# Optimization experiments

Hardware: AMD Instinct MI355X
Metric: run time of the kernel (lower is better)

The kernel has to match this reference:

```python
import jax, jax.numpy as jnp
import numpy as np

LN_EPS = 1e-5


def layer_norm(x, g, b):
    m = jnp.mean(x, axis=-1, keepdims=True)
    v = jnp.mean(jnp.square(x - m), axis=-1, keepdims=True)
    return (x - m) * jax.lax.rsqrt(v + LN_EPS) * g + b


def sym_norm(A):
    # D^{-1/2} (A + I) D^{-1/2}
    N = A.shape[0]
    Ah = A + jnp.eye(N, dtype=A.dtype)
    d = jnp.sum(Ah, axis=-1)
    dinv = jax.lax.rsqrt(jnp.maximum(d, 1e-12))
    return Ah * dinv[:, None] * dinv[None, :]


def gru_layer(xs, Wih, Whh, bih, bhh):
    # xs: (BN, T, Din) -> ys: (BN, T, H). PyTorch GRU cell math.
    BN, T, _ = xs.shape
    H = Whh.shape[1]
    x_proj = xs @ Wih.T + bih  # (BN, T, 3H), precompute input projections

    def step(h, xp):
        hp = h @ Whh.T + bhh
        xr, xz, xn = jnp.split(xp, 3, axis=-1)
        hr, hz, hn = jnp.split(hp, 3, axis=-1)
        r = jax.nn.sigmoid(xr + hr)
        z = jax.nn.sigmoid(xz + hz)
        n = jnp.tanh(xn + r * hn)
        h_new = (1.0 - z) * n + z * h
        return h_new, h_new

    h0 = jnp.zeros((BN, H), xs.dtype)
    _, ys = jax.lax.scan(step, h0, jnp.swapaxes(x_proj, 0, 1))
    return jnp.swapaxes(ys, 0, 1)


def amscf_forward(x, A, FSP, DSP,
                  E1, E2, fus_W, fus_b, fus_v, beta1, beta2,
                  gcn_W1, gcn_b1, ln1_g, ln1_b, gcn_W2, gcn_b2, ln2_g, ln2_b,
                  gru_Wih0, gru_Whh0, gru_bih0, gru_bhh0,
                  gru_Wih1, gru_Whh1, gru_bih1, gru_bhh1,
                  att_w, fc1_W, fc1_b, fc2_W, fc2_b):
    B, T, N, _ = x.shape
    Hor = fc2_W.shape[0]

    # ImprovedAdjacency: blend A with adaptive node-embedding adjacency
    Aadp = jax.nn.softmax(jax.nn.relu(E1 @ E2.T), axis=-1)
    IA = 0.5 * A + 0.5 * Aadp

    # fuse_with_A with learned gates
    w1 = jax.nn.sigmoid(beta1)
    w2 = jax.nn.sigmoid(beta2)
    C1 = w1 * A + (1.0 - w1) * FSP
    C2 = w2 * A + (1.0 - w2) * DSP

    # TransposeAttentionFusion: graph-level attention over the 3 candidate graphs
    Gs = jnp.stack([IA, C1, C2], axis=0)  # (3, N, N)
    sc = jnp.mean(jnp.tanh(Gs @ fus_W.T + fus_b) @ fus_v, axis=-1)  # (3,)
    alpha = jax.nn.softmax(sc)
    MG = jnp.einsum('k,knm->nm', alpha, Gs)

    S_hat = sym_norm(MG)  # (N, N)

    # TwoLayerGCN over all (B, T) at once: act(LN(S X W1)) -> LN(S h W2)
    xf = x.reshape(B * T, N, 1)
    h = jnp.einsum('mn,bnc->bmc', S_hat, xf) @ gcn_W1 + gcn_b1
    h = jax.nn.relu(layer_norm(h, ln1_g, ln1_b))
    g = jnp.einsum('mn,bnc->bmc', S_hat, h) @ gcn_W2 + gcn_b2
    g = layer_norm(g, ln2_g, ln2_b)  # (B*T, N, C)

    C = g.shape[-1]
    # Faithful to original: raw view of (B, T, N, C) into (B*N, T, C)
    H_seq = g.reshape(B, T, N, C).reshape(B * N, T, C)

    out = gru_layer(H_seq, gru_Wih0, gru_Whh0, gru_bih0, gru_bhh0)
    out = gru_layer(out, gru_Wih1, gru_Whh1, gru_bih1, gru_bhh1)  # (BN, T, Hg)

    # SoftAttentionPooling over time
    score = out @ att_w  # (BN, T)
    att = jax.nn.softmax(score, axis=1)
    ctx = jnp.einsum('bt,bth->bh', att, out)

    hfc = jax.nn.gelu(ctx @ fc1_W.T + fc1_b)
    dlt = hfc @ fc2_W.T + fc2_b  # (BN, Hor); dropout is identity at eval
    return jnp.transpose(dlt.reshape(B, N, Hor), (0, 2, 1))  # (B, Hor, N)


def setup_inputs() -> dict:
    B, T, N, Hor = 32, 12, 1000, 12
    Cin, Ch, Cout, Hg, Da, De = 1, 96, 96, 192, 32, 10
    key = jax.random.key(0)
    ks = jax.random.split(key, 32)
    f32 = jnp.float32

    def nrm(k, shape, scale):
        return jax.random.normal(k, shape, dtype=f32) * scale

    inp = {
        'x': jax.random.normal(ks[0], (B, T, N, Cin), dtype=f32),
        'A': jax.random.uniform(ks[1], (N, N), dtype=f32),
        'FSP': jax.random.uniform(ks[2], (N, N), dtype=f32),
        'DSP': jax.random.uniform(ks[3], (N, N), dtype=f32),
        'E1': nrm(ks[4], (N, De), 0.1),
        'E2': nrm(ks[5], (N, De), 0.1),
        'fus_W': nrm(ks[6], (Da, N), 1.0 / np.sqrt(N)),
        'fus_b': jnp.zeros((Da,), f32),
        'fus_v': nrm(ks[7], (Da,), 1.0 / np.sqrt(Da)),
        'beta1': jnp.float32(0.5),
        'beta2': jnp.float32(0.5),
        'gcn_W1': nrm(ks[8], (Cin, Ch), 1.0 / np.sqrt(Cin)),
        'gcn_b1': jnp.zeros((Ch,), f32),
        'ln1_g': jnp.ones((Ch,), f32),
        'ln1_b': jnp.zeros((Ch,), f32),
        'gcn_W2': nrm(ks[9], (Ch, Cout), 1.0 / np.sqrt(Ch)),
        'gcn_b2': jnp.zeros((Cout,), f32),
        'ln2_g': jnp.ones((Cout,), f32),
        'ln2_b': jnp.zeros((Cout,), f32),
        'gru_Wih0': nrm(ks[10], (3 * Hg, Cout), 1.0 / np.sqrt(Hg)),
        'gru_Whh0': nrm(ks[11], (3 * Hg, Hg), 1.0 / np.sqrt(Hg)),
        'gru_bih0': jnp.zeros((3 * Hg,), f32),
        'gru_bhh0': jnp.zeros((3 * Hg,), f32),
        'gru_Wih1': nrm(ks[12], (3 * Hg, Hg), 1.0 / np.sqrt(Hg)),
        'gru_Whh1': nrm(ks[13], (3 * Hg, Hg), 1.0 / np.sqrt(Hg)),
        'gru_bih1': jnp.zeros((3 * Hg,), f32),
        'gru_bhh1': jnp.zeros((3 * Hg,), f32),
        'att_w': nrm(ks[14], (Hg,), 1.0 / np.sqrt(Hg)),
        'fc1_W': nrm(ks[15], (Hg, Hg), 1.0 / np.sqrt(Hg)),
        'fc1_b': jnp.zeros((Hg,), f32),
        'fc2_W': nrm(ks[16], (Hor, Hg), 1.0 / np.sqrt(Hg)),
        'fc2_b': jnp.zeros((Hor,), f32),
    }
    return inp


def reference(x, A, FSP, DSP, E1, E2, fus_W, fus_b, fus_v, beta1, beta2,
              gcn_W1, gcn_b1, ln1_g, ln1_b, gcn_W2, gcn_b2, ln2_g, ln2_b,
              gru_Wih0, gru_Whh0, gru_bih0, gru_bhh0,
              gru_Wih1, gru_Whh1, gru_bih1, gru_bhh1,
              att_w, fc1_W, fc1_b, fc2_W, fc2_b):
    return amscf_forward(x, A, FSP, DSP, E1, E2, fus_W, fus_b, fus_v, beta1, beta2,
                         gcn_W1, gcn_b1, ln1_g, ln1_b, gcn_W2, gcn_b2, ln2_g, ln2_b,
                         gru_Wih0, gru_Whh0, gru_bih0, gru_bhh0,
                         gru_Wih1, gru_Whh1, gru_bih1, gru_bhh1,
                         att_w, fc1_W, fc1_b, fc2_W, fc2_b)
```

## Files before the change

### kernel.cpp

```cpp
#include <hip/hip_runtime.h>

typedef unsigned short u16;
typedef unsigned int u32;
typedef __attribute__((ext_vector_type(8))) short short8;
typedef __attribute__((ext_vector_type(4))) float float4v;

#define DEV static __device__ __forceinline__

DEV float bf2f(u16 u) { u32 x = ((u32)u) << 16; float f; __builtin_memcpy(&f, &x, 4); return f; }
DEV u16 f2bf(float f) {
  u32 u; __builtin_memcpy(&u, &f, 4);
  u = (u + 0x7fffu + ((u >> 16) & 1u)) >> 16;
  return (u16)u;
}
DEV float sigm(float x) { return 1.f / (1.f + __expf(-x)); }

DEV void gl16(const u16* g, u16* l) {
  __builtin_amdgcn_global_load_lds(
      (const __attribute__((address_space(1))) void*)g,
      (__attribute__((address_space(3))) void*)l, 16, 0, 0);
}

template <int OMODE>
__launch_bounds__(256)
__global__ void gemm_nt(const u16* __restrict__ A, int lda,
                        const u16* __restrict__ B, int ldb,
                        void* __restrict__ Cp, int ldc,
                        int M, int N, int K,
                        const float* __restrict__ bias)
{
  constexpr int PK = 40;
  __shared__ u16 As[128 * PK];
  __shared__ u16 Bs[64 * PK];

  const int tid  = threadIdx.x;
  const int m0   = blockIdx.y * 128;
  const int n0   = blockIdx.x * 64;
  const int wid  = tid >> 6;
  const int lane = tid & 63;
  const int l15  = lane & 15;
  const int quad = lane >> 4;
  const int wm   = (wid >> 1) * 64;
  const int wn   = (wid & 1) * 32;

  float4v acc[4][2];
  const float4v fz = {0.f, 0.f, 0.f, 0.f};
#pragma unroll
  for (int i = 0; i < 4; i++)
#pragma unroll
    for (int j = 0; j < 2; j++) acc[i][j] = fz;

  const int arow = tid >> 2;
  const int akc  = tid & 3;

  const int kt_count = (K + 31) / 32;
  for (int kt = 0; kt < kt_count; ++kt) {
    const int k0 = kt * 32 + akc * 8;
    const bool kok = (k0 < K);
    uint4 av0 = make_uint4(0, 0, 0, 0), av1 = av0, bv = av0;
    int ra = m0 + arow;
    if (kok && ra < M)        av0 = *(const uint4*)(A + (size_t)ra * lda + k0);
    if (kok && ra + 64 < M)   av1 = *(const uint4*)(A + (size_t)(ra + 64) * lda + k0);
    int rb = n0 + arow;
    if (kok && rb < N)        bv  = *(const uint4*)(B + (size_t)rb * ldb + k0);

    __syncthreads();
    *(uint4*)&As[arow * PK + akc * 8]        = av0;
    *(uint4*)&As[(arow + 64) * PK + akc * 8] = av1;
    *(uint4*)&Bs[arow * PK + akc * 8]        = bv;
    __syncthreads();

    short8 af[4], bfr[2];
#pragma unroll
    for (int i = 0; i < 4; i++)
      af[i] = *(const short8*)&As[(wm + i * 16 + l15) * PK + quad * 8];
#pragma unroll
    for (int j = 0; j < 2; j++)
      bfr[j] = *(const short8*)&Bs[(wn + j * 16 + l15) * PK + quad * 8];
#pragma unroll
    for (int i = 0; i < 4; i++)
#pragma unroll
      for (int j = 0; j < 2; j++)
        acc[i][j] = __builtin_amdgcn_mfma_f32_16x16x32_bf16(af[i], bfr[j], acc[i][j], 0, 0, 0);
  }

#pragma unroll
  for (int i = 0; i < 4; i++)
#pragma unroll
    for (int j = 0; j < 2; j++)
#pragma unroll
      for (int e = 0; e < 4; e++) {
        int r = m0 + wm + i * 16 + quad * 4 + e;
        int c = n0 + wn + j * 16 + l15;
        if (r < M && c < N) {
          float v = acc[i][j][e];
          if (OMODE == 0) ((float*)Cp)[(size_t)r * ldc + c] = v;
          else {
            float a = v + bias[c];
            float t = tanhf(0.7978845608028654f * (a + 0.044715f * a * a * a));
            ((float*)Cp)[(size_t)r * ldc + c] = 0.5f * a * (1.f + t);
          }
        }
      }
}

__launch_bounds__(256)
__global__ void k_bigemm(const u16* __restrict__ A,
                         const u16* __restrict__ B,
                         const float* __restrict__ b2, const float* __restrict__ g2,
                         const float* __restrict__ be2,
                         u16* __restrict__ Gg)
{
  __shared__ u16 As[128 * 32];
  __shared__ u16 Bs[96 * 32];
  __shared__ float stats[2][2][128];

  const int tid  = threadIdx.x;
  const int bid  = blockIdx.x;
  const int xcd  = bid & 7;
  const int jj   = bid >> 3;
  const int m0   = (jj & 7) * 128;
  const int rt   = xcd + 8 * (jj >> 3);

  const int wid  = tid >> 6;
  const int lane = tid & 63;
  const int l15  = lane & 15;
  const int quad = lane >> 4;
  const int wm   = (wid >> 1) * 64;
  const int wn   = (wid & 1) * 48;
  const int wni  = wid & 1;

  const int srow = lane >> 2;
  const int skc  = ((lane & 3) ^ ((lane >> 3) & 3)) * 8;

  const u16* agp0 = A + (size_t)(m0 + wid * 16 + srow) * 1024 + skc;
  const u16* agp1 = agp0 + (size_t)64 * 1024;
  const u16* bgp0 = B + (size_t)(rt * 96 + wid * 16 + srow) * 1024 + skc;
  const u16* bgp1 = bgp0 + (size_t)64 * 1024;
  u16* asl0 = &As[(wid * 16) * 32];
  u16* asl1 = &As[(64 + wid * 16) * 32];
  u16* bsl0 = &Bs[(wid * 16) * 32];
  u16* bsl1 = &Bs[(64 + wid * 16) * 32];

  float4v acc[4][3];
  const float4v fz = {0.f, 0.f, 0.f, 0.f};
#pragma unroll
  for (int i = 0; i < 4; i++)
#pragma unroll
    for (int j = 0; j < 3; j++) acc[i][j] = fz;

  const int swa = (quad ^ ((l15 >> 1) & 3)) * 8;

  for (int kt = 0; kt < 32; ++kt) {
    const int ko = kt * 32;
    gl16(agp0 + ko, asl0);
    gl16(agp1 + ko, asl1);
    gl16(bgp0 + ko, bsl0);
    if (wid < 2) gl16(bgp1 + ko, bsl1);
    __syncthreads();
    short8 af[4], bf[3];
#pragma unroll
    for (int i = 0; i < 4; i++)
      af[i] = *(const short8*)&As[(wm + i * 16 + l15) * 32 + swa];
#pragma unroll
    for (int j = 0; j < 3; j++)
      bf[j] = *(const short8*)&Bs[(wn + j * 16 + l15) * 32 + swa];
#pragma unroll
    for (int i = 0; i < 4; i++)
#pragma unroll
      for (int j = 0; j < 3; j++)
        acc[i][j] = __builtin_amdgcn_mfma_f32_16x16x32_bf16(af[i], bf[j], acc[i][j], 0, 0, 0);
    __syncthreads();
  }

  float b2v[3], g2v[3], bev[3];
#pragma unroll
  for (int j = 0; j < 3; j++) {
    int c = wn + j * 16 + l15;
    b2v[j] = b2[c]; g2v[j] = g2[c]; bev[j] = be2[c];
  }
#pragma unroll
  for (int i = 0; i < 4; i++)
#pragma unroll
    for (int e = 0; e < 4; e++) {
      float s = 0.f, ss = 0.f;
#pragma unroll
      for (int j = 0; j < 3; j++) {
        float v = acc[i][j][e] + b2v[j];
        acc[i][j][e] = v;
        s += v; ss += v * v;
      }
      s += __shfl_xor(s, 1); ss += __shfl_xor(ss, 1);
      s += __shfl_xor(s, 2); ss += __shfl_xor(ss, 2);
      s += __shfl_xor(s, 4); ss += __shfl_xor(ss, 4);
      s += __shfl_xor(s, 8); ss += __shfl_xor(ss, 8);
      if (l15 == 0) {
        int rl = wm + i * 16 + quad * 4 + e;
        stats[wni][0][rl] = s;
        stats[wni][1][rl] = ss;
      }
    }
  __syncthreads();
#pragma unroll
  for (int i = 0; i < 4; i++)
#pragma unroll
    for (int e = 0; e < 4; e++) {
      int rl = wm + i * 16 + quad * 4 + e;
      int m = m0 + rl;
      if (m < 1000) {
        float ts  = stats[0][0][rl] + stats[1][0][rl];
        float tss = stats[0][1][rl] + stats[1][1][rl];
        float mean = ts * (1.f / 96.f);
        float var  = tss * (1.f / 96.f) - mean * mean;
        float isd  = rsqrtf(var + 1e-5f);
#pragma unroll
        for (int j = 0; j < 3; j++) {
          int c = wn + j * 16 + l15;
          Gg[(size_t)rt * 96000 + (size_t)m * 96 + c] =
              f2bf((acc[i][j][e] - mean) * isd * g2v[j] + bev[j]);
        }
      }
    }
}

template <int KX, bool POOL>
__launch_bounds__(256)
__global__ void k_gru(const u16* __restrict__ Xin, int ldx,
                      const u16* __restrict__ Win,
                      const u16* __restrict__ Hin,
                      const u16* __restrict__ Whh,
                      const float* __restrict__ bih, const float* __restrict__ bhh,
                      u16* __restrict__ Hout,
                      const float* __restrict__ att_w,
                      float* __restrict__ score_acc,
                      float* __restrict__ score_zero,
                      const u16* __restrict__ Hpool,
                      const float* __restrict__ score_rd,
                      const float* __restrict__ Mrd, const float* __restrict__ Lrd,
                      float* __restrict__ Mwr, float* __restrict__ Lwr,
                      float* __restrict__ Nvp,
                      int t0, int pm)
{
  __shared__ u16 As[128 * 64];
  __shared__ u16 Bs[96 * 64];
  const int tid  = threadIdx.x;
  const int m0   = blockIdx.y * 128;
  const int c0   = blockIdx.x * 32;
  const int wid  = tid >> 6;
  const int lane = tid & 63;
  const int l15  = lane & 15;
  const int quad = lane >> 4;
  const int wm   = wid * 32;

  if (!POOL && pm) {
#pragma unroll
    for (int k = 0; k < 16; k++) {
      int idx = k * 256 + tid;
      int ql = idx >> 5, cl = idx & 31;
      int q = m0 + ql, c = c0 + cl;
      size_t nidx = (size_t)q * 192 + c;
      float s = score_rd[q];
      float hnew = bf2f(Hpool[nidx]);
      float so, wnf, prev;
      if (pm == 1) { so = 0.f; wnf = 1.f; prev = 0.f; }
      else {
        float Mo = Mrd[q];
        float Mn = fmaxf(Mo, s);
        so = __expf(Mo - Mn); wnf = __expf(s - Mn);
        prev = Nvp[nidx];
      }
      Nvp[nidx] = prev * so + wnf * hnew;
    }
    if (blockIdx.x == 0 && tid < 128) {
      int q = m0 + tid;
      float s = score_rd[q];
      if (pm == 1) { Mwr[q] = s; Lwr[q] = 1.f; }
      else {
        float Mo = Mrd[q], Mn = fmaxf(Mo, s);
        Mwr[q] = Mn;
        Lwr[q] = Lrd[q] * __expf(Mo - Mn) + __expf(s - Mn);
      }
    }
  }
  if (POOL && blockIdx.x == 0 && tid < 128) score_zero[m0 + tid] = 0.f;

  const int srow8 = lane >> 3;
  const int sw8   = ((lane & 7) ^ srow8) * 8;
  const int srow4 = lane >> 2;
  const int sw4   = ((lane & 3) ^ ((lane >> 3) & 3)) * 8;

  float4v aR[2][2], aZ[2][2], aXN[2][2], aHN[2][2];
  const float4v fz = {0.f, 0.f, 0.f, 0.f};
#pragma unroll
  for (int i = 0; i < 2; i++)
#pragma unroll
    for (int j = 0; j < 2; j++) { aR[i][j] = fz; aZ[i][j] = fz; aXN[i][j] = fz; aHN[i][j] = fz; }

  if (KX == 96) {
    const u16* ax0 = Xin + (size_t)(m0 + wid * 16 + srow4) * ldx + sw4;
    const u16* ax1 = Xin + (size_t)(m0 + 64 + wid * 16 + srow4) * ldx + sw4;
    const int b0 = wid * 16 + srow4;
    const u16* bx0 = Win + (size_t)((b0 >> 5) * 192 + c0 + (b0 & 31)) * 96 + sw4;
    const int b1 = 64 + wid * 16 + srow4;
    const u16* bx1 = Win + (size_t)(384 + c0 + (b1 & 31)) * 96 + sw4;
    u16* asl0 = &As[(wid * 16) * 32];
    u16* asl1 = &As[(64 + wid * 16) * 32];
    u16* bsl0 = &Bs[(wid * 16) * 32];
    u16* bsl1 = &Bs[(64 + wid * 16) * 32];
    const int swa = (quad ^ ((l15 >> 1) & 3)) * 8;
#pragma unroll
    for (int kt = 0; kt < 3; ++kt) {
      const int ko = kt * 32;
      gl16(ax0 + ko, asl0); gl16(ax1 + ko, asl1);
      gl16(bx0 + ko, bsl0);
      if (wid < 2) gl16(bx1 + ko, bsl1);
      __syncthreads();
      short8 af[2], bR[2], bZ[2], bN[2];
#pragma unroll
      for (int i = 0; i < 2; i++)
        af[i] = *(const short8*)&As[(wm + i * 16 + l15) * 32 + swa];
#pragma unroll
      for (int j = 0; j < 2; j++) {
        bR[j] = *(const short8*)&Bs[(j * 16 + l15) * 32 + swa];
        bZ[j] = *(const short8*)&Bs[(32 + j * 16 + l15) * 32 + swa];
        bN[j] = *(const short8*)&Bs[(64 + j * 16 + l15) * 32 + swa];
      }
#pragma unroll
      for (int i = 0; i < 2; i++)
#pragma unroll
        for (int j = 0; j < 2; j++) {
          aR[i][j]  = __builtin_amdgcn_mfma_f32_16x16x32_bf16(af[i], bR[j], aR[i][j], 0, 0, 0);
          aZ[i][j]  = __builtin_amdgcn_mfma_f32_16x16x32_bf16(af[i], bZ[j], aZ[i][j], 0, 0, 0);
          aXN[i][j] = __builtin_amdgcn_mfma_f32_16x16x32_bf16(af[i], bN[j], aXN[i][j], 0, 0, 0);
        }
      __syncthreads();
    }
  } else {
    const u16* abase = Xin + (size_t)(m0 + wid * 8 + srow8) * 192 + sw8;
    const u16* bbase = Win + (size_t)(c0 + wid * 8 + srow8) * 192 + sw8;
#pragma unroll
    for (int kt = 0; kt < 3; ++kt) {
      const int ko = kt * 64;
#pragma unroll
      for (int c = 0; c < 4; c++)
        gl16(abase + (size_t)c * 32 * 192 + ko, &As[(c * 32 + wid * 8) * 64]);
#pragma unroll
      for (int c = 0; c < 3; c++)
        gl16(bbase + (size_t)c * 192 * 192 + ko, &Bs[(c * 32 + wid * 8) * 64]);
      __syncthreads();
#pragma unroll
      for (int k32 = 0; k32 < 2; k32++) {
        const int swr = ((quad + 4 * k32) ^ (l15 & 7)) * 8;
        short8 af[2], bR[2], bZ[2], bN[2];
#pragma unroll
        for (int i = 0; i < 2; i++)
          af[i] = *(const short8*)&As[(wm + i * 16 + l15) * 64 + swr];
#pragma unroll
        for (int j = 0; j < 2; j++) {
          bR[j] = *(const short8*)&Bs[(j * 16 + l15) * 64 + swr];
          bZ[j] = *(const short8*)&Bs[(32 + j * 16 + l15) * 64 + swr];
          bN[j] = *(const short8*)&Bs[(64 + j * 16 + l15) * 64 + swr];
        }
#pragma unroll
        for (int i = 0; i < 2; i++)
#pragma unroll
          for (int j = 0; j < 2; j++) {
            aR[i][j]  = __builtin_amdgcn_mfma_f32_16x16x32_bf16(af[i], bR[j], aR[i][j], 0, 0, 0);
            aZ[i][j]  = __builtin_amdgcn_mfma_f32_16x16x32_bf16(af[i], bZ[j], aZ[i][j], 0, 0, 0);
            aXN[i][j] = __builtin_amdgcn_mfma_f32_16x16x32_bf16(af[i], bN[j], aXN[i][j], 0, 0, 0);
          }
      }
      __syncthreads();
    }
  }
  if (!t0) {
    const u16* abase = Hin + (size_t)(m0 + wid * 8 + srow8) * 192 + sw8;
    const u16* bbase = Whh + (size_t)(c0 + wid * 8 + srow8) * 192 + sw8;
#pragma unroll
    for (int kt = 0; kt < 3; ++kt) {
      const int ko = kt * 64;
#pragma unroll
      for (int c = 0; c < 4; c++)
        gl16(abase + (size_t)c * 32 * 192 + ko, &As[(c * 32 + wid * 8) * 64]);
#pragma unroll
      for (int c = 0; c < 3; c++)
        gl16(bbase + (size_t)c * 192 * 192 + ko, &Bs[(c * 32 + wid * 8) * 64]);
      __syncthreads();
#pragma unroll
      for (int k32 = 0; k32 < 2; k32++) {
        const int swr = ((quad + 4 * k32) ^ (l15 & 7)) * 8;
        short8 af[2], bR[2], bZ[2], bN[2];
#pragma unroll
        for (int i = 0; i < 2; i++)
          af[i] = *(const short8*)&As[(wm + i * 16 + l15) * 64 + swr];
#pragma unroll
        for (int j = 0; j < 2; j++) {
          bR[j] = *(const short8*)&Bs[(j * 16 + l15) * 64 + swr];
          bZ[j] = *(const short8*)&Bs[(32 + j * 16 + l15) * 64 + swr];
          bN[j] = *(const short8*)&Bs[(64 + j * 16 + l15) * 64 + swr];
        }
#pragma unroll
        for (int i = 0; i < 2; i++)
#pragma unroll
          for (int j = 0; j < 2; j++) {
            aR[i][j]  = __builtin_amdgcn_mfma_f32_16x16x32_bf16(af[i], bR[j], aR[i][j], 0, 0, 0);
            aZ[i][j]  = __builtin_amdgcn_mfma_f32_16x16x32_bf16(af[i], bZ[j], aZ[i][j], 0, 0, 0);
            aHN[i][j] = __builtin_amdgcn_mfma_f32_16x16x32_bf16(af[i], bN[j], aHN[i][j], 0, 0, 0);
          }
      }
      __syncthreads();
    }
  }

  float ps[2][4];
  if (POOL) {
#pragma unroll
    for (int i = 0; i < 2; i++)
#pragma unroll
      for (int e = 0; e < 4; e++) ps[i][e] = 0.f;
  }
#pragma unroll
  for (int j = 0; j < 2; ++j) {
    const int c = c0 + j * 16 + l15;
    const float brz = bih[c] + bhh[c];
    const float bzz = bih[192 + c] + bhh[192 + c];
    const float bxn = bih[384 + c];
    const float bhn = bhh[384 + c];
    const float aw  = POOL ? att_w[c] : 0.f;
#pragma unroll
    for (int i = 0; i < 2; ++i)
#pragma unroll
      for (int e = 0; e < 4; ++e) {
        const int row = m0 + wm + i * 16 + quad * 4 + e;
        float rg  = sigm(aR[i][j][e] + brz);
        float zg  = sigm(aZ[i][j][e] + bzz);
        float hnv = bhn + (t0 ? 0.f : aHN[i][j][e]);
        float ng  = tanhf(aXN[i][j][e] + bxn + rg * hnv);
        float hold = t0 ? 0.f : bf2f(Hin[(size_t)row * 192 + c]);
        float hnew = (1.f - zg) * ng + zg * hold;
        Hout[(size_t)row * 192 + c] = f2bf(hnew);
        if (POOL) ps[i][e] += hnew * aw;
      }
  }
  if (POOL) {
#pragma unroll
    for (int i = 0; i < 2; ++i)
#pragma unroll
      for (int e = 0; e < 4; ++e) {
        float v = ps[i][e];
        v += __shfl_xor(v, 1); v += __shfl_xor(v, 2);
        v += __shfl_xor(v, 4); v += __shfl_xor(v, 8);
        if (l15 == 0) atomicAdd(&score_acc[m0 + wm + i * 16 + quad * 4 + e], v);
      }
  }
}

__launch_bounds__(256)
__global__ void k_pool(const u16* __restrict__ H, const float* __restrict__ score_rd,
                       const float* __restrict__ Mrd, const float* __restrict__ Lrd,
                       float* __restrict__ Lwr, float* __restrict__ Nv)
{
  const int base = blockIdx.x * 1536;
  const int tid  = threadIdx.x;
#pragma unroll
  for (int k = 0; k < 6; k++) {
    const int idx = base + tid + k * 256;
    const int q = idx / 192;
    const float s = score_rd[q];
    const float Mo = Mrd[q];
    const float Mn = fmaxf(Mo, s);
    const float so = __expf(Mo - Mn);
    const float wn = __expf(s - Mn);
    Nv[idx] = Nv[idx] * so + wn * bf2f(H[idx]);
  }
  if (tid < 8) {
    const int q = blockIdx.x * 8 + tid;
    const float s = score_rd[q];
    const float Mo = Mrd[q];
    const float Mn = fmaxf(Mo, s);
    Lwr[q] = Lrd[q] * __expf(Mo - Mn) + __expf(s - Mn);
  }
}

__launch_bounds__(256)
__global__ void k_h2gemm(const float* __restrict__ yt, const float4* __restrict__ cwpk,
                         const u16* __restrict__ W2s, const float* __restrict__ consts,
                         u16* __restrict__ h2t)
{
  constexpr int PK = 40;
  __shared__ u16 As[128 * PK];
  __shared__ u16 Bs[96 * PK];
  __shared__ u16 Ts[96 * 136];

  const int tid  = threadIdx.x;
  const int m0   = blockIdx.x * 128;
  const int wid  = tid >> 6;
  const int lane = tid & 63;
  const int l15  = lane & 15;
  const int quad = lane >> 4;
  const int wm   = (wid >> 1) * 64;
  const int wn   = (wid & 1) * 48;

  const float P = consts[0], Q = consts[1], VW = consts[2], CWB = consts[3], VB = consts[4];

  const int arow = tid >> 2;
  const int akc  = tid & 3;

  float yv[2], mu[2], iv[2];
#pragma unroll
  for (int rr = 0; rr < 2; rr++) {
    int i = m0 + arow + rr * 64;
    int r = i / 1000, n = i - r * 1000;
    float y = yt[n * 384 + r];
    yv[rr] = y;
    mu[rr] = y * P + Q;
    iv[rr] = rsqrtf(y * y * VW + 2.f * y * CWB + VB + 1e-5f);
  }

  float4v acc[4][3];
  const float4v fz = {0.f, 0.f, 0.f, 0.f};
#pragma unroll
  for (int i = 0; i < 4; i++)
#pragma unroll
    for (int j = 0; j < 3; j++) acc[i][j] = fz;

  uint4 asave[2][3];
  const bool has2 = (arow < 32);

  for (int kt = 0; kt < 6; ++kt) {
    const int k0 = kt * 32 + akc * 8;
    uint4 av[2];
    if (kt < 3) {
#pragma unroll
      for (int rr = 0; rr < 2; rr++) {
        u16 hb[8];
#pragma unroll
        for (int e = 0; e < 8; e++) {
          float4 cw = cwpk[k0 + e];
          float t = yv[rr] * cw.x + cw.y - mu[rr];
          float h = fmaxf(t * iv[rr] * cw.z + cw.w, 0.f);
          hb[e] = f2bf(h);
        }
        __builtin_memcpy(&av[rr], hb, 16);
        asave[rr][kt] = av[rr];
      }
    } else {
      av[0] = asave[0][kt - 3];
      av[1] = asave[1][kt - 3];
    }
    uint4 bv0 = *(const uint4*)(W2s + (size_t)arow * 192 + k0);
    uint4 bv1 = make_uint4(0, 0, 0, 0);
    if (has2) bv1 = *(const uint4*)(W2s + (size_t)(arow + 64) * 192 + k0);

    __syncthreads();
    *(uint4*)&As[arow * PK + akc * 8]        = av[0];
    *(uint4*)&As[(arow + 64) * PK + akc * 8] = av[1];
    *(uint4*)&Bs[arow * PK + akc * 8]        = bv0;
    if (has2) *(uint4*)&Bs[(arow + 64) * PK + akc * 8] = bv1;
    __syncthreads();

    short8 af[4], bfr[3];
#pragma unroll
    for (int i = 0; i < 4; i++)
      af[i] = *(const short8*)&As[(wm + i * 16 + l15) * PK + quad * 8];
#pragma unroll
    for (int j = 0; j < 3; j++)
      bfr[j] = *(const short8*)&Bs[(wn + j * 16 + l15) * PK + quad * 8];
#pragma unroll
    for (int i = 0; i < 4; i++)
#pragma unroll
      for (int j = 0; j < 3; j++)
        acc[i][j] = __builtin_amdgcn_mfma_f32_16x16x32_bf16(af[i], bfr[j], acc[i][j], 0, 0, 0);
  }

#pragma unroll
  for (int i = 0; i < 4; i++)
#pragma unroll
    for (int j = 0; j < 3; j++)
#pragma unroll
      for (int e = 0; e < 4; e++) {
        int rowl = wm + i * 16 + quad * 4 + e;
        int c2   = wn + j * 16 + l15;
        Ts[c2 * 136 + rowl] = f2bf(acc[i][j][e]);
      }
  __syncthreads();
#pragma unroll
  for (int u = tid; u < 1536; u += 256) {
    int c2 = u >> 4, ch = u & 15;
    int iidx0 = m0 + ch * 8;
    int r = iidx0 / 1000, n0 = iidx0 - r * 1000;
    *(uint4*)(h2t + (size_t)(r * 96 + c2) * 1024 + n0) = *(const uint4*)&Ts[c2 * 136 + ch * 8];
  }
}

__launch_bounds__(256)
__global__ void k_prep(const float* x, const float* fus_W,
                       const float* Wih0, const float* Whh0,
                       const float* Wih1, const float* Whh1,
                       const float* gcn_W1, const float* gcn_b1,
                       const float* gcn_W2, const float* ln1g, const float* ln1b,
                       u16* xbf, u16* fusWbf, u16* Wih0b, u16* Whh0b, u16* Wih1b, u16* Whh1b,
                       u16* W2s, float4* cwpk, float* consts)
{
  long o = (long)blockIdx.x * 256 + threadIdx.x;
  if (o < 384000) xbf[o] = f2bf(x[o]);
  else if ((o -= 384000) < 32000) fusWbf[o] = f2bf(fus_W[o]);
  else if ((o -= 32000) < 55296)  Wih0b[o] = f2bf(Wih0[o]);
  else if ((o -= 55296) < 110592) Whh0b[o] = f2bf(Whh0[o]);
  else if ((o -= 110592) < 110592) Wih1b[o] = f2bf(Wih1[o]);
  else if ((o -= 110592) < 110592) Whh1b[o] = f2bf(Whh1[o]);
  else if ((o -= 110592) < 9216) {
    int c2 = (int)o / 96, c = (int)o - c2 * 96;
    float wv = gcn_W2[c * 96 + c2];
    u16 hi = f2bf(wv);
    u16 lo = f2bf(wv - bf2f(hi));
    W2s[c2 * 192 + c] = hi;
    W2s[c2 * 192 + 96 + c] = lo;
  }
  else if ((o -= 9216) < 96) {
    int c = (int)o;
    float4 cw;
    cw.x = gcn_W1[c]; cw.y = gcn_b1[c]; cw.z = ln1g[c]; cw.w = ln1b[c];
    cwpk[c] = cw;
  }
  if (blockIdx.x == 0 && threadIdx.x == 0) {
    float sw = 0, sb = 0, sww = 0, swb = 0, sbb = 0;
    for (int c = 0; c < 96; c++) {
      float wv = gcn_W1[c], b = gcn_b1[c];
      sw += wv; sb += b; sww += wv * wv; swb += wv * b; sbb += b * b;
    }
    float P = sw / 96.f, Q = sb / 96.f;
    consts[0] = P; consts[1] = Q;
    consts[2] = sww / 96.f - P * P;
    consts[3] = swb / 96.f - P * Q;
    consts[4] = sbb / 96.f - Q * Q;
  }
}

__launch_bounds__(256)
__global__ void k_zero(u16* __restrict__ h2t, float* __restrict__ score0,
                       float* __restrict__ score1)
{
  int idx = blockIdx.x * 256 + threadIdx.x;
  if (idx < 110592) {
    int row = idx / 3, p = idx - row * 3;
    *(uint4*)(h2t + (size_t)row * 1024 + 1000 + p * 8) = make_uint4(0, 0, 0, 0);
  } else if ((idx -= 110592) < 32000) {
    score0[idx] = 0.f;
  } else if ((idx -= 32000) < 32000) {
    score1[idx] = 0.f;
  }
}

__launch_bounds__(256)
__global__ void k_w1split(const float* __restrict__ fc1W, u16* __restrict__ w1s)
{
  int idx = blockIdx.x * 256 + threadIdx.x;
  if (idx >= 192 * 192) return;
  int n = idx / 192, k = idx - n * 192;
  float w = fc1W[idx];
  u16 hi = f2bf(w);
  u16 lo = f2bf(w - bf2f(hi));
  w1s[(size_t)n * 576 + k]       = hi;
  w1s[(size_t)n * 576 + 192 + k] = lo;
  w1s[(size_t)n * 576 + 384 + k] = hi;
}

__launch_bounds__(256)
__global__ void k_adjrow(const float* __restrict__ A, const float* __restrict__ FSP,
                         const float* __restrict__ DSP, const float* __restrict__ E1,
                         const float* __restrict__ E2,
                         const float* beta1, const float* beta2,
                         u16* __restrict__ G, float* __restrict__ rowsums)
{
  __shared__ float z[1000];
  __shared__ float red[256];
  const int n = blockIdx.x, tid = threadIdx.x;

  float e1r[10];
#pragma unroll
  for (int d = 0; d < 10; d++) e1r[d] = E1[n * 10 + d];

  float lmax = -1e30f;
  for (int m = tid; m < 1000; m += 256) {
    float s = 0;
#pragma unroll
    for (int d = 0; d < 10; d++) s += e1r[d] * E2[m * 10 + d];
    s = fmaxf(s, 0.f);
    z[m] = s;
    lmax = fmaxf(lmax, s);
  }
  red[tid] = lmax; __syncthreads();
  for (int st = 128; st > 0; st >>= 1) { if (tid < st) red[tid] = fmaxf(red[tid], red[tid + st]); __syncthreads(); }
  const float mx = red[0]; __syncthreads();

  float lsum = 0;
  for (int m = tid; m < 1000; m += 256) { float e = __expf(z[m] - mx); z[m] = e; lsum += e; }
  red[tid] = lsum; __syncthreads();
  for (int st = 128; st > 0; st >>= 1) { if (tid < st) red[tid] += red[tid + st]; __syncthreads(); }
  const float inv = 1.f / red[0]; __syncthreads();

  const float w1 = sigm(beta1[0]);
  const float w2 = sigm(beta2[0]);
  float s0 = 0, s1 = 0, s2 = 0;
  for (int m = tid; m < 1000; m += 256) {
    float aadp = z[m] * inv;
    float a = A[n * 1000 + m], f = FSP[n * 1000 + m], dd = DSP[n * 1000 + m];
    float g0 = 0.5f * a + 0.5f * aadp;
    float g1 = w1 * a + (1.f - w1) * f;
    float g2 = w2 * a + (1.f - w2) * dd;
    G[0 * 1000000 + n * 1000 + m] = f2bf(g0);
    G[1 * 1000000 + n * 1000 + m] = f2bf(g1);
    G[2 * 1000000 + n * 1000 + m] = f2bf(g2);
    s0 += g0; s1 += g1; s2 += g2;
  }
  red[tid] = s0; __syncthreads();
  for (int st = 128; st > 0; st >>= 1) { if (tid < st) red[tid] += red[tid + st]; __syncthreads(); }
  if (tid == 0) rowsums[n] = red[0];
  __syncthreads();
  red[tid] = s1; __syncthreads();
  for (int st = 128; st > 0; st >>= 1) { if (tid < st) red[tid] += red[tid + st]; __syncthreads(); }
  if (tid == 0) rowsums[1000 + n] = red[0];
  __syncthreads();
  red[tid] = s2; __syncthreads();
  for (int st = 128; st > 0; st >>= 1) { if (tid < st) red[tid] += red[tid + st]; __syncthreads(); }
  if (tid == 0) rowsums[2000 + n] = red[0];
}

__launch_bounds__(256)
__global__ void k_sc(const float* __restrict__ P, const float* fus_b, const float* fus_v, float* sc)
{
  __shared__ float red[256];
  const int k = blockIdx.x, tid = threadIdx.x;
  float local = 0;
  for (int n = tid; n < 1000; n += 256) {
    const float* p = P + (size_t)(k * 1000 + n) * 32;
    float s = 0;
#pragma unroll
    for (int a = 0; a < 32; a++) s += tanhf(p[a] + fus_b[a]) * fus_v[a];
    local += s;
  }
  red[tid] = local; __syncthreads();
  for (int st = 128; st > 0; st >>= 1) { if (tid < st) red[tid] += red[tid + st]; __syncthreads(); }
  if (tid == 0) sc[k] = red[0] * (1.f / 1000.f);
}

__launch_bounds__(256)
__global__ void k_alpha(const float* sc, const float* rowsums, float* alpha_out, float* dinv)
{
  __shared__ float al[3];
  const int tid = threadIdx.x;
  if (tid == 0) {
    float m = fmaxf(sc[0], fmaxf(sc[1], sc[2]));
    float e0 = __expf(sc[0] - m), e1 = __expf(sc[1] - m), e2 = __expf(sc[2] - m);
    float inv = 1.f / (e0 + e1 + e2);
    al[0] = e0 * inv; al[1] = e1 * inv; al[2] = e2 * inv;
    alpha_out[0] = al[0]; alpha_out[1] = al[1]; alpha_out[2] = al[2];
  }
  __syncthreads();
  const float a0 = al[0], a1 = al[1], a2 = al[2];
  for (int n = tid; n < 1000; n += 256) {
    float d = a0 * rowsums[n] + a1 * rowsums[1000 + n] + a2 * rowsums[2000 + n] + 1.0f;
    dinv[n] = rsqrtf(fmaxf(d, 1e-12f));
  }
}

__launch_bounds__(256)
__global__ void k_shat(const u16* __restrict__ G, const float* alpha, const float* dinv,
                       u16* __restrict__ S)
{
  int idx = blockIdx.x * 256 + threadIdx.x;
  if (idx >= 1024000) return;
  int i = idx >> 10, j = idx & 1023;
  u16 val = 0;
  if (j < 1000) {
    const float a0 = alpha[0], a1 = alpha[1], a2 = alpha[2];
    int g = i * 1000 + j;
    float mg = a0 * bf2f(G[g]) + a1 * bf2f(G[1000000 + g]) + a2 * bf2f(G[2000000 + g]);
    if (i == j) mg += 1.0f;
    val = f2bf(mg * dinv[i] * dinv[j]);
  }
  S[(size_t)i * 1024 + j] = val;
}

__launch_bounds__(256)
__global__ void k_ctxsplit(const float* __restrict__ Nv, const float* __restrict__ Lbuf,
                           u16* __restrict__ ctxs)
{
  const int i = blockIdx.x * 256 + threadIdx.x;
  if (i >= 32000 * 192) return;
  const int q = i / 192, c = i - q * 192;
  float v = Nv[i] / Lbuf[q];
  u16 hi = f2bf(v);
  u16 lo = f2bf(v - bf2f(hi));
  u16* row = ctxs + (size_t)q * 576;
  row[c] = hi; row[192 + c] = hi; row[384 + c] = lo;
}

__launch_bounds__(192)
__global__ void k_fc2(const float* __restrict__ hfc, const float* __restrict__ fc2W,
                      const float* __restrict__ fc2b, float* __restrict__ out)
{
  __shared__ float w2S[12][193];
  __shared__ float hS[16][193];
  const int tid = threadIdx.x;
  const int q0 = blockIdx.x * 16;
  for (int idx = tid; idx < 12 * 192; idx += 192) {
    int o = idx / 192, k = idx - o * 192;
    w2S[o][k] = fc2W[idx];
  }
  for (int idx = tid; idx < 16 * 192; idx += 192) {
    int qq = idx / 192, k = idx - qq * 192;
    hS[qq][k] = hfc[(size_t)(q0 + qq) * 192 + k];
  }
  __syncthreads();
  const int qq = tid / 12, o = tid - qq * 12;
  float acc = fc2b[o];
#pragma unroll 8
  for (int k = 0; k < 192; k++) acc += hS[qq][k] * w2S[o][k];
  const int q = q0 + qq;
  const int b = q / 1000, node = q - b * 1000;
  out[(size_t)b * 12000 + o * 1000 + node] = acc;
}

extern "C" void kernel_launch(void* const* d_in, const int* in_sizes, int n_in,
                              void* d_out, int out_size, void* d_ws, size_t ws_size,
                              hipStream_t stream)
{
  const float* x     = (const float*)d_in[0];
  const float* A     = (const float*)d_in[1];
  const float* FSP   = (const float*)d_in[2];
  const float* DSP   = (const float*)d_in[3];
  const float* E1    = (const float*)d_in[4];
  const float* E2    = (const float*)d_in[5];
  const float* fus_W = (const float*)d_in[6];
  const float* fus_b = (const float*)d_in[7];
  const float* fus_v = (const float*)d_in[8];
  const float* beta1 = (const float*)d_in[9];
  const float* beta2 = (const float*)d_in[10];
  const float* gcn_W1= (const float*)d_in[11];
  const float* gcn_b1= (const float*)d_in[12];
  const float* ln1g  = (const float*)d_in[13];
  const float* ln1b  = (const float*)d_in[14];
  const float* gcn_W2= (const float*)d_in[15];
  const float* gcn_b2= (const float*)d_in[16];
  const float* ln2g  = (const float*)d_in[17];
  const float* ln2b  = (const float*)d_in[18];
  const float* Wih0  = (const float*)d_in[19];
  const float* Whh0  = (const float*)d_in[20];
  const float* bih0  = (const float*)d_in[21];
  const float* bhh0  = (const float*)d_in[22];
  const float* Wih1  = (const float*)d_in[23];
  const float* Whh1  = (const float*)d_in[24];
  const float* bih1  = (const float*)d_in[25];
  const float* bhh1  = (const float*)d_in[26];
  const float* att_w = (const float*)d_in[27];
  const float* fc1W  = (const float*)d_in[28];
  const float* fc1b  = (const float*)d_in[29];
  const float* fc2W  = (const float*)d_in[30];
  const float* fc2b  = (const float*)d_in[31];
  float* out = (float*)d_out;

  char* w = (char*)d_ws;
  auto alloc = [&](size_t bytes) -> char* {
    char* p = w;
    w += (bytes + 255) & ~(size_t)255;
    return p;
  };

  float* consts  = (float*)alloc(8 * 4);
  float* scp     = (float*)alloc(3 * 4);
  float* alphap  = (float*)alloc(3 * 4);
  float* rowsums = (float*)alloc(3000 * 4);
  float* dinvp   = (float*)alloc(1000 * 4);
  u16*   Gbuf    = (u16*)alloc((size_t)3000000 * 2);
  u16*   Sbf     = (u16*)alloc((size_t)1024 * 1024 * 2);
  u16*   xbf     = (u16*)alloc((size_t)384000 * 2);
  u16*   fusWbf  = (u16*)alloc((size_t)32000 * 2);
  u16*   Wih0b   = (u16*)alloc((size_t)55296 * 2);
  u16*   Whh0b   = (u16*)alloc((size_t)110592 * 2);
  u16*   Wih1b   = (u16*)alloc((size_t)110592 * 2);
  u16*   Whh1b   = (u16*)alloc((size_t)110592 * 2);
  u16*   w1s     = (u16*)alloc((size_t)192 * 576 * 2);
  u16*   W2s     = (u16*)alloc((size_t)96 * 192 * 2);
  float4* cwpk   = (float4*)alloc((size_t)96 * 16);
  float* Pbuf    = (float*)alloc((size_t)96000 * 4);
  float* yt      = (float*)alloc((size_t)384000 * 4);
  u16*   h2t     = (u16*)alloc((size_t)36864 * 1024 * 2);
  u16*   Gg      = (u16*)alloc((size_t)36864000 * 2);
  float* Nv      = (float*)alloc((size_t)6144000 * 4);
  float* Mb0     = (float*)alloc((size_t)32000 * 4);
  float* Mb1     = (float*)alloc((size_t)32000 * 4);
  float* Lb0     = (float*)alloc((size_t)32000 * 4);
  float* Lb1     = (float*)alloc((size_t)32000 * 4);
  float* sc0     = (float*)alloc((size_t)32000 * 4);
  float* sc1     = (float*)alloc((size_t)32000 * 4);
  float* Mbuf[2] = { Mb0, Mb1 };
  float* Lbuf[2] = { Lb0, Lb1 };
  float* score[2]= { sc0, sc1 };

  u16* h0buf[2] = { h2t,                    h2t + (size_t)6144000 };
  u16* h1buf[2] = { h2t + (size_t)12288000, h2t + (size_t)18432000 };
  u16*   ctxs = h2t;
  float* hfc  = (float*)(h2t + (size_t)18432000);

  k_prep<<<3174, 256, 0, stream>>>(x, fus_W, Wih0, Whh0, Wih1, Whh1, gcn_W1, gcn_b1,
                                   gcn_W2, ln1g, ln1b,
                                   xbf, fusWbf, Wih0b, Whh0b, Wih1b, Whh1b, W2s, cwpk, consts);
  k_w1split<<<144, 256, 0, stream>>>(fc1W, w1s);
  k_zero<<<682, 256, 0, stream>>>(h2t, sc0, sc1);
  k_adjrow<<<1000, 256, 0, stream>>>(A, FSP, DSP, E1, E2, beta1, beta2, Gbuf, rowsums);
  gemm_nt<0><<<dim3(1, 24), 256, 0, stream>>>(Gbuf, 1000, fusWbf, 1000, Pbuf, 32, 3000, 32, 1000, nullptr);
  k_sc<<<3, 256, 0, stream>>>(Pbuf, fus_b, fus_v, scp);
  k_alpha<<<1, 256, 0, stream>>>(scp, rowsums, alphap, dinvp);
  k_shat<<<4000, 256, 0, stream>>>(Gbuf, alphap, dinvp, Sbf);
  gemm_nt<0><<<dim3(6, 8), 256, 0, stream>>>(Sbf, 1024, xbf, 1000, yt, 384, 1000, 384, 1000, nullptr);
  k_h2gemm<<<3000, 256, 0, stream>>>(yt, cwpk, W2s, consts, h2t);
  k_bigemm<<<3072, 256, 0, stream>>>(Sbf, h2t, gcn_b2, ln2g, ln2b, Gg);

  for (int t = 0; t < 12; ++t) {
    u16* h0in  = h0buf[t & 1];
    u16* h0out = h0buf[(t & 1) ^ 1];
    u16* h1in  = h1buf[t & 1];
    u16* h1out = h1buf[(t & 1) ^ 1];
    const int pm = (t == 0) ? 0 : (t == 1 ? 1 : 2);
    k_gru<96, false><<<dim3(6, 250), 256, 0, stream>>>(
        Gg + t * 96, 1152, Wih0b, h0in, Whh0b, bih0, bhh0, h0out,
        nullptr, nullptr, nullptr,
        h1in, score[(t + 1) & 1],
        Mbuf[(t + 1) & 1], Lbuf[(t + 1) & 1], Mbuf[t & 1], Lbuf[t & 1],
        Nv, t == 0, pm);
    k_gru<192, true><<<dim3(6, 250), 256, 0, stream>>>(
        h0out, 192, Wih1b, h1in, Whh1b, bih1, bhh1, h1out,
        att_w, score[t & 1], score[(t + 1) & 1],
        nullptr, nullptr, nullptr, nullptr, nullptr, nullptr, nullptr,
        t == 0, 0);
  }
  k_pool<<<4000, 256, 0, stream>>>(h1buf[0], score[1], Mbuf[1], Lbuf[1], Lbuf[0], Nv);

  k_ctxsplit<<<24000, 256, 0, stream>>>(Nv, Lbuf[0], ctxs);
  gemm_nt<3><<<dim3(3, 250), 256, 0, stream>>>(ctxs, 576, w1s, 576, hfc, 192, 32000, 192, 576, fc1b);
  k_fc2<<<2000, 192, 0, stream>>>(hfc, fc2W, fc2b, out);
}
```

Baseline: 1.520 ms.

## Fuse GRU time loop into persistent cooperative kernel and widen bigemm K tile

Replaces the 24 per-timestep GRU kernel launches with one cooperative persistent kernel. It runs 1024 blocks that loop over the tiles of each layer and separate the phases with grid-wide syncs, keeping a fallback to the old launches if the cooperative launch fails. Separately, the big GCN GEMM now stages 64-wide K tiles instead of 32, halving the loop trips and barriers at the cost of more shared memory. Risks: the grid sync itself costs time, the occupancy hint of 4 blocks per CU may not hold for 1024 blocks, and the new code references Mb0/Lb0/sc0 host variables that must already exist.

```diff
diff --git a/kernel.cpp b/kernel.cpp
--- a/kernel.cpp
+++ b/kernel.cpp
@@ -1,4 +1,7 @@
 #include <hip/hip_runtime.h>
+#include <hip/hip_cooperative_groups.h>
+
+namespace cg = cooperative_groups;
 
 typedef unsigned short u16;
 typedef unsigned int u32;
@@ -111,8 +114,8 @@
                          const float* __restrict__ be2,
                          u16* __restrict__ Gg)
 {
-  __shared__ u16 As[128 * 32];
-  __shared__ u16 Bs[96 * 32];
+  __shared__ u16 As[128 * 64];
+  __shared__ u16 Bs[96 * 64];
   __shared__ float stats[2][2][128];
 
   const int tid  = threadIdx.x;
@@ -130,17 +133,11 @@
   const int wn   = (wid & 1) * 48;
   const int wni  = wid & 1;
 
-  const int srow = lane >> 2;
-  const int skc  = ((lane & 3) ^ ((lane >> 3) & 3)) * 8;
-
-  const u16* agp0 = A + (size_t)(m0 + wid * 16 + srow) * 1024 + skc;
-  const u16* agp1 = agp0 + (size_t)64 * 1024;
-  const u16* bgp0 = B + (size_t)(rt * 96 + wid * 16 + srow) * 1024 + skc;
-  const u16* bgp1 = bgp0 + (size_t)64 * 1024;
-  u16* asl0 = &As[(wid * 16) * 32];
-  u16* asl1 = &As[(64 + wid * 16) * 32];
-  u16* bsl0 = &Bs[(wid * 16) * 32];
-  u16* bsl1 = &Bs[(64 + wid * 16) * 32];
+  const int srow8 = lane >> 3;
+  const int sw8   = ((lane & 7) ^ srow8) * 8;
+
+  const u16* abase = A + (size_t)(m0 + wid * 8 + srow8) * 1024 + sw8;
+  const u16* bbase = B + (size_t)(rt * 96 + wid * 8 + srow8) * 1024 + sw8;
 
   float4v acc[4][3];
   const float4v fz = {0.f, 0.f, 0.f, 0.f};
@@ -149,27 +146,31 @@
 #pragma unroll
     for (int j = 0; j < 3; j++) acc[i][j] = fz;
 
-  const int swa = (quad ^ ((l15 >> 1) & 3)) * 8;
-
-  for (int kt = 0; kt < 32; ++kt) {
-    const int ko = kt * 32;
-    gl16(agp0 + ko, asl0);
-    gl16(agp1 + ko, asl1);
-    gl16(bgp0 + ko, bsl0);
-    if (wid < 2) gl16(bgp1 + ko, bsl1);
+  for (int kt = 0; kt < 16; ++kt) {
+    const int ko = kt * 64;
+#pragma unroll
+    for (int c = 0; c < 4; c++)
+      gl16(abase + (size_t)c * 32 * 1024 + ko, &As[(c * 32 + wid * 8) * 64]);
+#pragma unroll
+    for (int c = 0; c < 3; c++)
+      gl16(bbase + (size_t)c * 32 * 1024 + ko, &Bs[(c * 32 + wid * 8) * 64]);
     __syncthreads();
-    short8 af[4], bf[3];
-#pragma unroll
-    for (int i = 0; i < 4; i++)
-      af[i] = *(const short8*)&As[(wm + i * 16 + l15) * 32 + swa];
-#pragma unroll
-    for (int j = 0; j < 3; j++)
-      bf[j] = *(const short8*)&Bs[(wn + j * 16 + l15) * 32 + swa];
-#pragma unroll
-    for (int i = 0; i < 4; i++)
+#pragma unroll
+    for (int k32 = 0; k32 < 2; k32++) {
+      const int swr = ((quad + 4 * k32) ^ (l15 & 7)) * 8;
+      short8 af[4], bf[3];
+#pragma unroll
+      for (int i = 0; i < 4; i++)
+        af[i] = *(const short8*)&As[(wm + i * 16 + l15) * 64 + swr];
 #pragma unroll
       for (int j = 0; j < 3; j++)
-        acc[i][j] = __builtin_amdgcn_mfma_f32_16x16x32_bf16(af[i], bf[j], acc[i][j], 0, 0, 0);
+        bf[j] = *(const short8*)&Bs[(wn + j * 16 + l15) * 64 + swr];
+#pragma unroll
+      for (int i = 0; i < 4; i++)
+#pragma unroll
+        for (int j = 0; j < 3; j++)
+          acc[i][j] = __builtin_amdgcn_mfma_f32_16x16x32_bf16(af[i], bf[j], acc[i][j], 0, 0, 0);
+    }
     __syncthreads();
   }
 
@@ -224,28 +225,25 @@
 }
 
 template <int KX, bool POOL>
-__launch_bounds__(256)
-__global__ void k_gru(const u16* __restrict__ Xin, int ldx,
-                      const u16* __restrict__ Win,
-                      const u16* __restrict__ Hin,
-                      const u16* __restrict__ Whh,
-                      const float* __restrict__ bih, const float* __restrict__ bhh,
-                      u16* __restrict__ Hout,
-                      const float* __restrict__ att_w,
-                      float* __restrict__ score_acc,
-                      float* __restrict__ score_zero,
-                      const u16* __restrict__ Hpool,
-                      const float* __restrict__ score_rd,
-                      const float* __restrict__ Mrd, const float* __restrict__ Lrd,
-                      float* __restrict__ Mwr, float* __restrict__ Lwr,
-                      float* __restrict__ Nvp,
-                      int t0, int pm)
-{
-  __shared__ u16 As[128 * 64];
-  __shared__ u16 Bs[96 * 64];
+DEV void gru_tile(u16* As, u16* Bs,
+                  int m0, int c0,
+                  const u16* __restrict__ Xin, int ldx,
+                  const u16* __restrict__ Win,
+                  const u16* __restrict__ Hin,
+                  const u16* __restrict__ Whh,
+                  const float* __restrict__ bih, const float* __restrict__ bhh,
+                  u16* __restrict__ Hout,
+                  const float* __restrict__ att_w,
+                  float* __restrict__ score_acc,
+                  float* __restrict__ score_zero,
+                  const u16* __restrict__ Hpool,
+                  const float* __restrict__ score_rd,
+                  const float* __restrict__ Mrd, const float* __restrict__ Lrd,
+                  float* __restrict__ Mwr, float* __restrict__ Lwr,
+                  float* __restrict__ Nvp,
+                  int t0, int pm)
+{
   const int tid  = threadIdx.x;
-  const int m0   = blockIdx.y * 128;
-  const int c0   = blockIdx.x * 32;
   const int wid  = tid >> 6;
   const int lane = tid & 63;
   const int l15  = lane & 15;
@@ -271,7 +269,7 @@
       }
       Nvp[nidx] = prev * so + wnf * hnew;
     }
-    if (blockIdx.x == 0 && tid < 128) {
+    if (c0 == 0 && tid < 128) {
       int q = m0 + tid;
       float s = score_rd[q];
       if (pm == 1) { Mwr[q] = s; Lwr[q] = 1.f; }
@@ -282,7 +280,7 @@
       }
     }
   }
-  if (POOL && blockIdx.x == 0 && tid < 128) score_zero[m0 + tid] = 0.f;
+  if (POOL && c0 == 0 && tid < 128) score_zero[m0 + tid] = 0.f;
 
   const int srow8 = lane >> 3;
   const int sw8   = ((lane & 7) ^ srow8) * 8;
@@ -452,6 +450,71 @@
         v += __shfl_xor(v, 4); v += __shfl_xor(v, 8);
         if (l15 == 0) atomicAdd(&score_acc[m0 + wm + i * 16 + quad * 4 + e], v);
       }
+  }
+}
+
+template <int KX, bool POOL>
+__launch_bounds__(256)
+__global__ void k_gru(const u16* __restrict__ Xin, int ldx,
+                      const u16* __restrict__ Win,
+                      const u16* __restrict__ Hin,
+                      const u16* __restrict__ Whh,
+                      const float* __restrict__ bih, const float* __restrict__ bhh,
+                      u16* __restrict__ Hout,
+                      const float* __restrict__ att_w,
+                      float* __restrict__ score_acc, float* __restrict__ score_zero,
+                      const u16* __restrict__ Hpool, const float* __restrict__ score_rd,
+                      const float* __restrict__ Mrd, const float* __restrict__ Lrd,
+                      float* __restrict__ Mwr, float* __restrict__ Lwr,
+                      float* __restrict__ Nvp, int t0, int pm)
+{
+  __shared__ u16 As[128 * 64];
+  __shared__ u16 Bs[96 * 64];
+  gru_tile<KX, POOL>(As, Bs, blockIdx.y * 128, blockIdx.x * 32,
+                     Xin, ldx, Win, Hin, Whh, bih, bhh, Hout, att_w,
+                     score_acc, score_zero, Hpool, score_rd, Mrd, Lrd, Mwr, Lwr, Nvp, t0, pm);
+}
+
+struct GruArgs {
+  const u16 *Gg, *Wih0, *Whh0, *Wih1, *Whh1;
+  const float *bih0, *bhh0, *bih1, *bhh1, *att_w;
+  u16 *h0a, *h0b, *h1a, *h1b;
+  float *M0, *M1, *L0, *L1, *s0, *s1;
+  float* Nv;
+};
+
+__launch_bounds__(256, 4)
+__global__ void k_grup(GruArgs a)
+{
+  __shared__ u16 As[128 * 64];
+  __shared__ u16 Bs[96 * 64];
+  cg::grid_group grid = cg::this_grid();
+  u16* h0buf[2] = { a.h0a, a.h0b };
+  u16* h1buf[2] = { a.h1a, a.h1b };
+  float* Mb[2] = { a.M0, a.M1 };
+  float* Lb[2] = { a.L0, a.L1 };
+  float* sc[2] = { a.s0, a.s1 };
+
+  for (int t = 0; t < 12; ++t) {
+    const int pm = (t == 0) ? 0 : (t == 1 ? 1 : 2);
+    for (int tile = blockIdx.x; tile < 1500; tile += gridDim.x) {
+      int m0 = (tile % 250) * 128, c0 = (tile / 250) * 32;
+      gru_tile<96, false>(As, Bs, m0, c0,
+          a.Gg + t * 96, 1152, a.Wih0, h0buf[t & 1], a.Whh0, a.bih0, a.bhh0, h0buf[(t & 1) ^ 1],
+          nullptr, nullptr, nullptr,
+          h1buf[t & 1], sc[(t + 1) & 1], Mb[(t + 1) & 1], Lb[(t + 1) & 1],
+          Mb[t & 1], Lb[t & 1], a.Nv, t == 0, pm);
+    }
+    grid.sync();
+    for (int tile = blockIdx.x; tile < 1500; tile += gridDim.x) {
+      int m0 = (tile % 250) * 128, c0 = (tile / 250) * 32;
+      gru_tile<192, true>(As, Bs, m0, c0,
+          h0buf[(t & 1) ^ 1], 192, a.Wih1, h1buf[t & 1], a.Whh1, a.bih1, a.bhh1, h1buf[(t & 1) ^ 1],
+          a.att_w, sc[t & 1], sc[(t + 1) & 1],
+          nullptr, nullptr, nullptr, nullptr, nullptr, nullptr, nullptr,
+          t == 0, 0);
+    }
+    grid.sync();
   }
 }
 
@@ -918,23 +981,34 @@
   k_h2gemm<<<3000, 256, 0, stream>>>(yt, cwpk, W2s, consts, h2t);
   k_bigemm<<<3072, 256, 0, stream>>>(Sbf, h2t, gcn_b2, ln2g, ln2b, Gg);
 
-  for (int t = 0; t < 12; ++t) {
-    u16* h0in  = h0buf[t & 1];
-    u16* h0out = h0buf[(t & 1) ^ 1];
-    u16* h1in  = h1buf[t & 1];
-    u16* h1out = h1buf[(t & 1) ^ 1];
-    const int pm = (t == 0) ? 0 : (t == 1 ? 1 : 2);
-    k_gru<96, false><<<dim3(6, 250), 256, 0, stream>>>(
-        Gg + t * 96, 1152, Wih0b, h0in, Whh0b, bih0, bhh0, h0out,
-        nullptr, nullptr, nullptr,
-        h1in, score[(t + 1) & 1],
-        Mbuf[(t + 1) & 1], Lbuf[(t + 1) & 1], Mbuf[t & 1], Lbuf[t & 1],
-        Nv, t == 0, pm);
-    k_gru<192, true><<<dim3(6, 250), 256, 0, stream>>>(
-        h0out, 192, Wih1b, h1in, Whh1b, bih1, bhh1, h1out,
-        att_w, score[t & 1], score[(t + 1) & 1],
-        nullptr, nullptr, nullptr, nullptr, nullptr, nullptr, nullptr,
-        t == 0, 0);
+  GruArgs ga;
+  ga.Gg = Gg; ga.Wih0 = Wih0b; ga.Whh0 = Whh0b; ga.Wih1 = Wih1b; ga.Whh1 = Whh1b;
+  ga.bih0 = bih0; ga.bhh0 = bhh0; ga.bih1 = bih1; ga.bhh1 = bhh1; ga.att_w = att_w;
+  ga.h0a = h0buf[0]; ga.h0b = h0buf[1]; ga.h1a = h1buf[0]; ga.h1b = h1buf[1];
+  ga.M0 = Mb0; ga.M1 = Mb1; ga.L0 = Lb0; ga.L1 = Lb1; ga.s0 = sc0; ga.s1 = sc1;
+  ga.Nv = Nv;
+  void* kargs[] = { (void*)&ga };
+  hipError_t cerr = hipLaunchCooperativeKernel((void*)k_grup, dim3(1024), dim3(256),
+                                               kargs, 0, stream);
+  if (cerr != hipSuccess) {
+    for (int t = 0; t < 12; ++t) {
+      u16* h0in  = h0buf[t & 1];
+      u16* h0out = h0buf[(t & 1) ^ 1];
+      u16* h1in  = h1buf[t & 1];
+      u16* h1out = h1buf[(t & 1) ^ 1];
+      const int pm = (t == 0) ? 0 : (t == 1 ? 1 : 2);
+      k_gru<96, false><<<dim3(6, 250), 256, 0, stream>>>(
+          Gg + t * 96, 1152, Wih0b, h0in, Whh0b, bih0, bhh0, h0out,
+          nullptr, nullptr, nullptr,
+          h1in, score[(t + 1) & 1],
+          Mbuf[(t + 1) & 1], Lbuf[(t + 1) & 1], Mbuf[t & 1], Lbuf[t & 1],
+          Nv, t == 0, pm);
+      k_gru<192, true><<<dim3(6, 250), 256, 0, stream>>>(
+          h0out, 192, Wih1b, h1in, Whh1b, bih1, bhh1, h1out,
+          att_w, score[t & 1], score[(t + 1) & 1],
+          nullptr, nullptr, nullptr, nullptr, nullptr, nullptr, nullptr,
+          t == 0, 0);
+    }
   }
   k_pool<<<4000, 256, 0, stream>>>(h1buf[0], score[1], Mbuf[1], Lbuf[1], Lbuf[0], Nv);
 
```

New measurement: 4.651 ms. +205.9%, slower.
